# Kernel tuning notes

Measured on AMD Instinct MI355X. Metric: run time of the kernel, lower is better.

## Reference

```python
import jax, jax.numpy as jnp
import numpy as np

F = 15          # features
H = 128         # hidden_features
L = 12          # num_layers
NB = 16         # num_bins
M = 3 * NB - 1  # 47 params per feature (tails='linear')
TAIL = 3.0
MIN_W = 1e-3; MIN_H = 1e-3; MIN_D = 1e-3
B = 65536


def _masks():
    # nflows MADE sequential degrees
    deg_in = np.arange(1, F + 1)                       # input degrees 1..F
    deg_h = np.arange(H) % (F - 1) + 1                 # hidden degrees
    m_init = (deg_h[:, None] >= deg_in[None, :]).astype(np.float32)  # [H,F]
    m_h = (deg_h[:, None] >= deg_h[None, :]).astype(np.float32)      # [H,H]
    deg_out = np.repeat(deg_in, M)                     # tile -> repeat_interleave, [F*M]
    m_out = (deg_out[:, None] > deg_h[None, :]).astype(np.float32)   # [F*M,H], strict for output
    return jnp.asarray(m_init), jnp.asarray(m_h), jnp.asarray(m_out)


def setup_inputs() -> dict:
    key = jax.random.key(0)
    ks = jax.random.split(key, 7)
    s = 0.05
    return {
        "x": jax.random.normal(ks[0], (B, F), jnp.float32),
        "W_init": jax.random.normal(ks[1], (L, H, F), jnp.float32) * s,
        "b_init": jax.random.normal(ks[2], (L, H), jnp.float32) * s,
        "W_res": jax.random.normal(ks[3], (L, 2, 2, H, H), jnp.float32) * s,
        "b_res": jax.random.normal(ks[4], (L, 2, 2, H), jnp.float32) * s,
        "W_out": jax.random.normal(ks[5], (L, F * M, H), jnp.float32) * s,
        "b_out": jax.random.normal(ks[6], (L, F * M), jnp.float32) * s,
    }


def _made(x, p, m_init, m_h, m_out):
    # MADE with 2 masked residual blocks (relu, no BN/dropout), as in nflows
    h = x @ (p["W_init"] * m_init).T + p["b_init"]
    for blk in range(2):
        t = jax.nn.relu(h)
        t = t @ (p["W_res"][blk, 0] * m_h).T + p["b_res"][blk, 0]
        t = jax.nn.relu(t)
        t = t @ (p["W_res"][blk, 1] * m_h).T + p["b_res"][blk, 1]
        h = h + t
    return h @ (p["W_out"] * m_out).T + p["b_out"]  # [B, F*M]


def _rqs_forward(x, params):
    # unconstrained rational-quadratic spline, tails='linear' (nflows)
    uw = params[..., :NB]
    uh = params[..., NB:2 * NB]
    ud = params[..., 2 * NB:]                          # [B,F,NB-1]
    const = float(np.log(np.exp(1.0 - MIN_D) - 1.0))
    ud = jnp.pad(ud, ((0, 0), (0, 0), (1, 1)), constant_values=const)  # [B,F,NB+1]

    inside = (x >= -TAIL) & (x <= TAIL)
    xc = jnp.clip(x, -TAIL, TAIL)

    w = jax.nn.softmax(uw, axis=-1)
    w = MIN_W + (1.0 - MIN_W * NB) * w
    cw = jnp.pad(jnp.cumsum(w, axis=-1), ((0, 0), (0, 0), (1, 0)))
    cw = 2.0 * TAIL * cw - TAIL
    cw = cw.at[..., 0].set(-TAIL).at[..., -1].set(TAIL)
    w = cw[..., 1:] - cw[..., :-1]

    hgt = jax.nn.softmax(uh, axis=-1)
    hgt = MIN_H + (1.0 - MIN_H * NB) * hgt
    ch = jnp.pad(jnp.cumsum(hgt, axis=-1), ((0, 0), (0, 0), (1, 0)))
    ch = 2.0 * TAIL * ch - TAIL
    ch = ch.at[..., 0].set(-TAIL).at[..., -1].set(TAIL)
    hgt = ch[..., 1:] - ch[..., :-1]

    d = MIN_D + jax.nn.softplus(ud)                    # [B,F,NB+1]

    idx = jnp.clip(jnp.sum((xc[..., None] >= cw).astype(jnp.int32), axis=-1) - 1, 0, NB - 1)[..., None]
    g = lambda a: jnp.take_along_axis(a, idx, axis=-1)[..., 0]

    in_cw, in_w, in_ch, in_h = g(cw), g(w), g(ch), g(hgt)
    in_delta = g(hgt / w)
    in_d, in_d1 = g(d), g(d[..., 1:])

    theta = (xc - in_cw) / in_w
    tomt = theta * (1.0 - theta)
    num = in_h * (in_delta * theta ** 2 + in_d * tomt)
    den = in_delta + (in_d + in_d1 - 2.0 * in_delta) * tomt
    y = in_ch + num / den
    dnum = in_delta ** 2 * (in_d1 * theta ** 2 + 2.0 * in_delta * tomt + in_d * (1.0 - theta) ** 2)
    lad = jnp.log(dnum) - 2.0 * jnp.log(den)

    y = jnp.where(inside, y, x)                        # identity tails
    lad = jnp.where(inside, lad, 0.0)
    return y, jnp.sum(lad, axis=-1)


def reference(x, W_init, b_init, W_res, b_res, W_out, b_out):
    m_init, m_h, m_out = _masks()
    params = {"W_init": W_init, "b_init": b_init, "W_res": W_res,
              "b_res": b_res, "W_out": W_out, "b_out": b_out}

    def step(carry, p):
        xx, ld = carry
        xx = xx[:, ::-1]                               # ReversePermutation
        raw = _made(xx, p, m_init, m_h, m_out)
        xx, lad = _rqs_forward(xx, raw.reshape(xx.shape[0], F, M))
        return (xx, ld + lad), None

    (z, logdet), _ = jax.lax.scan(step, (x, jnp.zeros(x.shape[0], x.dtype)), params)
    return z, logdet
```

## Files before the change

kernel.cpp:

```cpp
#include <hip/hip_runtime.h>
#include <hip/hip_bf16.h>

#define FDIM 15
#define HDIM 128
#define LNUM 12
#define NBINS 16
#define MDIM 47
#define FM 705
#define BATCH 65536
#define TAILF 3.0f
#define MIN_Wc 0.001f
#define MIN_Hc 0.001f
#define MIN_Dc 0.001f

typedef __bf16 bf16_t;
typedef __attribute__((ext_vector_type(8))) __bf16 bf16x8;
typedef __attribute__((ext_vector_type(4))) __bf16 bf16x4;
typedef __attribute__((ext_vector_type(4))) float f32x4;

#define FRAGS_USED 211
#define FRAGS_PAD 224
#define FRAG_ELEMS 512
#define RING 16
#define WFRAG_TOTAL (LNUM * FRAGS_PAD * FRAG_ELEMS)

#define BB_FLOATS 1360
#define BB_TOTAL (LNUM * BB_FLOATS)

#define SPW 32

__device__ __forceinline__ int perm_pos(int pos) {
    int r, o;
    if (pos < 20) { r = pos / 10; o = pos % 10; }
    else          { r = 2 + (pos - 20) / 9; o = (pos - 20) % 9; }
    return r + 14 * o;
}

__device__ __forceinline__ float sp_softplus(float u) {
    return (u > 20.f) ? u : __logf(1.f + __expf(u));
}

__global__ void preproc_kernel(const float* __restrict__ Wi,
                               const float* __restrict__ Wr,
                               const float* __restrict__ Wo,
                               const float* __restrict__ bIg,
                               const float* __restrict__ bRg,
                               const float* __restrict__ bOg,
                               bf16_t* __restrict__ wfrag,
                               float* __restrict__ bblob) {
    const int RES_OFF[8] = {0, 1, 3, 5, 8, 11, 15, 19};
    const int OUT_OFF[15] = {0, 0, 3, 6, 9, 15, 21, 27, 36, 45, 54, 63, 75, 87, 99};
    const int OUT_CNT[15] = {0, 1, 1, 1, 2, 2, 2, 3, 3, 3, 3, 4, 4, 4, 4};

    int idx = blockIdx.x * blockDim.x + threadIdx.x;
    if (idx >= WFRAG_TOTAL) {
        int t = idx - WFRAG_TOTAL;
        if (t >= BB_TOTAL) return;
        int l = t / BB_FLOATS, r = t % BB_FLOATS;
        float v;
        if (r < 128) v = bIg[l * HDIM + perm_pos(r)];
        else if (r < 640) {
            int mat = (r - 128) >> 7, pos = (r - 128) & 127;
            v = bRg[(l * 4 + mat) * HDIM + perm_pos(pos)];
        } else {
            int q = r - 640, f = q / 48, j = q % 48;
            v = (j < 47) ? bOg[(size_t)l * FM + f * MDIM + j] : 0.f;
        }
        bblob[t] = v;
        return;
    }
    int j = idx & 7;
    int lane = (idx >> 3) & 63;
    int fg = idx >> 9;
    int g = fg % FRAGS_PAD;
    int l = fg / FRAGS_PAD;
    int quad = lane >> 4, n16 = lane & 15;
    int kk = quad * 8 + j;
    float val = 0.f;
    if (g < 8) {
        int n_orig = perm_pos(g * 16 + n16);
        if (kk < FDIM && (n_orig % 14) >= kk)
            val = Wi[(l * HDIM + n_orig) * FDIM + kk];
    } else if (g < 100) {
        int gg = g - 8;
        int mat = gg / 23, r = gg % 23;
        int mt = 7;
        while (mt > 0 && RES_OFF[mt] > r) mt--;
        int s = r - RES_OFF[mt];
        int j_orig = perm_pos(mt * 16 + n16);
        int k_orig = perm_pos(s * 32 + kk);
        if ((j_orig % 14) >= (k_orig % 14))
            val = Wr[((size_t)(l * 4 + mat) * HDIM + j_orig) * HDIM + k_orig];
    } else if (g < 211) {
        int gg = g - 100;
        int f = 14;
        while (f > 1 && OUT_OFF[f] > gg) f--;
        int q = gg - OUT_OFF[f];
        int cnt = OUT_CNT[f];
        int ty = q / cnt, s = q % cnt;
        int k_orig = perm_pos(s * 32 + kk);
        int o = (ty < 2) ? (f * MDIM + ty * 16 + n16)
                         : ((n16 < 15) ? (f * MDIM + 32 + n16) : -1);
        if (o >= 0 && f > (k_orig % 14))
            val = Wo[((size_t)l * FM + o) * HDIM + k_orig];
    }
    wfrag[idx] = (bf16_t)val;
}

__global__ __launch_bounds__(64, 2) void flow_kernel(
    const float* __restrict__ xin,
    float* __restrict__ zout,
    float* __restrict__ ldout,
    const bf16_t* __restrict__ wfrag,
    const float* __restrict__ bblob) {

    constexpr int RES_CNT_C[8] = {1, 2, 2, 3, 3, 4, 4, 4};
    constexpr int OUT_CNT_C[15] = {0, 1, 1, 1, 2, 2, 2, 3, 3, 3, 3, 4, 4, 4, 4};

    __shared__ __align__(16) float xs[SPW * 17];
    __shared__ __align__(16) unsigned char uni[13312];

    const int ln = threadIdx.x;
    const int quad = ln >> 4, n16 = ln & 15;
    const int fi = ln & 1, srow = ln >> 1;
    const int sbase = blockIdx.x * SPW;

    bf16_t* Bst = (bf16_t*)uni;
    float*  raw = (float*)uni;

    for (int t = ln; t < SPW * FDIM; t += 64) {
        int s = t / FDIM, c = t % FDIM;
        xs[s * 17 + c] = xin[(size_t)sbase * FDIM + t];
    }

    const bf16_t* wl = wfrag;
    bf16x8 Q[RING];
#pragma unroll
    for (int j = 0; j < RING; j++)
        Q[j] = *((const bf16x8*)(wl + (size_t)j * FRAG_ELEMS) + ln);

    float lad_sum = 0.f;
    bf16x8 bf[2][4];
    f32x4 h[2][8];

#pragma unroll 1
    for (int l = 0; l < LNUM; l++) {
        const float* bias = bblob + l * BB_FLOATS;

        float xc_pre[8];
#pragma unroll
        for (int p = 0; p < 8; p++) {
            int f = 2 * p + fi;
            xc_pre[p] = xs[srow * 17 + ((f < FDIM) ? (14 - f) : 0)];
        }
        bf16x8 a0[2];
#pragma unroll
        for (int T = 0; T < 2; T++)
#pragma unroll
            for (int j = 0; j < 8; j++) {
                int k = quad * 8 + j;
                a0[T][j] = (bf16_t)((k < FDIM) ? xs[(T * 16 + n16) * 17 + 14 - k] : 0.f);
            }

        int fp = 0;
        auto ldfrag = [&]() -> bf16x8 {
            bf16x8 r = Q[fp & (RING - 1)];
            Q[fp & (RING - 1)] =
                *((const bf16x8*)(wl + (size_t)(fp + RING) * FRAG_ELEMS) + ln);
            fp++;
            return r;
        };

        auto packmt = [&](int mt, f32x4 c0, f32x4 c1, bool relu) {
#pragma unroll
            for (int T = 0; T < 2; T++) {
                f32x4 c = T ? c1 : c0;
                bf16x4 pk;
#pragma unroll
                for (int r2 = 0; r2 < 4; r2++) {
                    float v = c[r2];
                    if (relu) v = fmaxf(v, 0.f);
                    pk[r2] = (bf16_t)v;
                }
                *(bf16x4*)&Bst[(T * 16 + n16) * 136 + mt * 16 + quad * 4] = pk;
            }
        };
        auto readbf = [&]() {
#pragma unroll
            for (int T = 0; T < 2; T++)
#pragma unroll
                for (int s = 0; s < 4; s++)
                    bf[T][s] = *(const bf16x8*)&Bst[(T * 16 + n16) * 136 + s * 32 + quad * 8];
        };

#pragma unroll
        for (int mt = 0; mt < 8; mt++) {
            f32x4 bbv = *(const f32x4*)&bias[mt * 16 + quad * 4];
            bf16x8 wf = ldfrag();
            f32x4 c0 = __builtin_amdgcn_mfma_f32_16x16x32_bf16(wf, a0[0], bbv, 0, 0, 0);
            f32x4 c1 = __builtin_amdgcn_mfma_f32_16x16x32_bf16(wf, a0[1], bbv, 0, 0, 0);
            h[0][mt] = c0; h[1][mt] = c1;
            packmt(mt, c0, c1, true);
        }
        readbf();

        auto gemm_pack = [&](const float* bm, bool addto, bool relu) {
#pragma unroll
            for (int mt = 0; mt < 8; mt++) {
                f32x4 bbv = *(const f32x4*)&bm[mt * 16 + quad * 4];
                f32x4 acc0 = addto ? (h[0][mt] + bbv) : bbv;
                f32x4 acc1 = addto ? (h[1][mt] + bbv) : bbv;
#pragma unroll
                for (int s = 0; s < RES_CNT_C[mt]; s++) {
                    bf16x8 wf = ldfrag();
                    acc0 = __builtin_amdgcn_mfma_f32_16x16x32_bf16(wf, bf[0][s], acc0, 0, 0, 0);
                    acc1 = __builtin_amdgcn_mfma_f32_16x16x32_bf16(wf, bf[1][s], acc1, 0, 0, 0);
                }
                if (addto) { h[0][mt] = acc0; h[1][mt] = acc1; }
                packmt(mt, acc0, acc1, relu);
            }
            readbf();
        };

        gemm_pack(bias + 128 + 0 * HDIM, false, true);
        gemm_pack(bias + 128 + 1 * HDIM, true,  true);
        gemm_pack(bias + 128 + 2 * HDIM, false, true);
        gemm_pack(bias + 128 + 3 * HDIM, true,  false);

        const float* bO48 = bias + 640;

#pragma unroll
        for (int p = 0; p < 8; p++) {
            const int nf = (p < 7) ? 2 : 1;
#pragma unroll
            for (int ff = 0; ff < 2; ff++) {
                if (ff >= nf) break;
                const int f = 2 * p + ff;
                const int cnt = OUT_CNT_C[f];
#pragma unroll
                for (int ty = 0; ty < 3; ty++) {
                    f32x4 acc0 = *(const f32x4*)&bO48[f * 48 + ty * 16 + quad * 4];
                    f32x4 acc1 = acc0;
#pragma unroll
                    for (int s = 0; s < cnt; s++) {
                        bf16x8 wf = ldfrag();
                        acc0 = __builtin_amdgcn_mfma_f32_16x16x32_bf16(wf, bf[0][s], acc0, 0, 0, 0);
                        acc1 = __builtin_amdgcn_mfma_f32_16x16x32_bf16(wf, bf[1][s], acc1, 0, 0, 0);
                    }
                    *(f32x4*)&raw[(ff * 32 + n16) * 52 + ty * 16 + quad * 4] = acc0;
                    *(f32x4*)&raw[(ff * 32 + 16 + n16) * 52 + ty * 16 + quad * 4] = acc1;
                }
            }

            if (fi < nf) {
                int f = 2 * p + fi;
                const float* rp = &raw[(fi * 32 + srow) * 52];
                float xr = xc_pre[p];
                bool inside = (xr >= -TAILF) && (xr <= TAILF);
                float xcv = fminf(fmaxf(xr, -TAILF), TAILF);

                float uw[NBINS], uh[NBINS];
                {
                    f32x4 v0 = *(const f32x4*)(rp + 0);
                    f32x4 v1 = *(const f32x4*)(rp + 4);
                    f32x4 v2 = *(const f32x4*)(rp + 8);
                    f32x4 v3 = *(const f32x4*)(rp + 12);
                    f32x4 w0 = *(const f32x4*)(rp + 16);
                    f32x4 w1 = *(const f32x4*)(rp + 20);
                    f32x4 w2 = *(const f32x4*)(rp + 24);
                    f32x4 w3 = *(const f32x4*)(rp + 28);
#pragma unroll
                    for (int i = 0; i < 4; i++) {
                        uw[i] = v0[i]; uw[4 + i] = v1[i]; uw[8 + i] = v2[i]; uw[12 + i] = v3[i];
                        uh[i] = w0[i]; uh[4 + i] = w1[i]; uh[8 + i] = w2[i]; uh[12 + i] = w3[i];
                    }
                }
                float mw = -1e30f, mh = -1e30f;
#pragma unroll
                for (int i = 0; i < NBINS; i++) {
                    mw = fmaxf(mw, uw[i]); mh = fmaxf(mh, uh[i]);
                }
                float swv = 0.f, shv = 0.f;
#pragma unroll
                for (int i = 0; i < NBINS; i++) {
                    uw[i] = __expf(uw[i] - mw); swv += uw[i];
                    uh[i] = __expf(uh[i] - mh); shv += uh[i];
                }
                float isw = (1.f - NBINS * MIN_Wc) / swv;
                float ish = (1.f - NBINS * MIN_Hc) / shv;

                float cumw = 0.f, cumh = 0.f;
                float left = -TAILF, chl_run = -TAILF;
                float lw = -TAILF, wsel = 1.f, chl = -TAILF, hsel = 1.f;
                int idx = 0;
#pragma unroll
                for (int b = 0; b < NBINS; b++) {
                    float wb = MIN_Wc + uw[b] * isw;
                    float hb = MIN_Hc + uh[b] * ish;
                    cumw += wb; cumh += hb;
                    float cwr = (b == NBINS - 1) ? TAILF : 2.f * TAILF * cumw - TAILF;
                    float chr = (b == NBINS - 1) ? TAILF : 2.f * TAILF * cumh - TAILF;
                    bool inb = (xcv >= left) && ((xcv < cwr) || (b == NBINS - 1));
                    if (inb) { idx = b; lw = left; wsel = cwr - left; chl = chl_run; hsel = chr - chl_run; }
                    left = cwr; chl_run = chr;
                }
                float d0 = 1.f, d1 = 1.f;
                if (idx > 0) d0 = MIN_Dc + sp_softplus(rp[2 * NBINS + idx - 1]);
                if (idx < NBINS - 1) d1 = MIN_Dc + sp_softplus(rp[2 * NBINS + idx]);

                float delta = hsel / wsel;
                float th = (xcv - lw) / wsel;
                float omt = 1.f - th;
                float tomt = th * omt;
                float num = hsel * (delta * th * th + d0 * tomt);
                float den = delta + (d0 + d1 - 2.f * delta) * tomt;
                float y = chl + num / den;
                float dnum = delta * delta * (d1 * th * th + 2.f * delta * tomt + d0 * omt * omt);
                float lad = __logf(dnum) - 2.f * __logf(den);

                y = inside ? y : xr;
                lad = inside ? lad : 0.f;
                xs[srow * 17 + f] = y;
                lad_sum += lad;
            }
        }

#pragma unroll
        for (int d = 0; d < FRAGS_PAD - FRAGS_USED; d++) {
            (void)ldfrag();
        }

        wl += (size_t)FRAGS_PAD * FRAG_ELEMS;
    }

    float v = lad_sum;
    v += __shfl_xor(v, 1);
    if (fi == 0) ldout[(size_t)sbase + srow] = v;

    for (int t = ln; t < SPW * FDIM; t += 64) {
        int s = t / FDIM, c = t % FDIM;
        zout[(size_t)sbase * FDIM + t] = xs[s * 17 + c];
    }
}

extern "C" void kernel_launch(void* const* d_in, const int* in_sizes, int n_in,
                              void* d_out, int out_size, void* d_ws, size_t ws_size,
                              hipStream_t stream) {
    const float* x  = (const float*)d_in[0];
    const float* Wi = (const float*)d_in[1];
    const float* bI = (const float*)d_in[2];
    const float* Wr = (const float*)d_in[3];
    const float* bR = (const float*)d_in[4];
    const float* Wo = (const float*)d_in[5];
    const float* bO = (const float*)d_in[6];

    bf16_t* wfrag = (bf16_t*)d_ws;
    size_t woff = ((size_t)WFRAG_TOTAL * 2 + (size_t)RING * FRAG_ELEMS * 2 + 255) & ~(size_t)255;
    float* bblob = (float*)((char*)d_ws + woff);
    float* zout  = (float*)d_out;
    float* ldout_final = zout + (size_t)BATCH * FDIM;

    const int totalP = WFRAG_TOTAL + BB_TOTAL;
    preproc_kernel<<<(totalP + 255) / 256, 256, 0, stream>>>(Wi, Wr, Wo, bI, bR, bO, wfrag, bblob);

    flow_kernel<<<BATCH / SPW, 64, 0, stream>>>(x, zout, ldout_final, wfrag, bblob);
}
```

Measured before the change: 413.2 us.

## Halve samples per block, shrink weight ring, and raise occupancy with 3-lane splines

Each block now handles 16 samples instead of 32. That halves the MFMA accumulator and activation registers, the weight prefetch ring shrinks from 16 to 8 fragments, and launch bounds allow 4 blocks per CU. The spline stage maps 4 lanes per sample, with 3 features per pass. Derivative parameters are preloaded into registers during bin search, and several divisions are replaced with hardware reciprocal. The aim is better latency hiding through occupancy, traded against twice the global weight-fragment traffic per sample and a shallower prefetch window.

Measured after the change: 775.2 us. 1.88x slower.

```diff
diff --git a/kernel.cpp b/kernel.cpp
--- a/kernel.cpp
+++ b/kernel.cpp
@@ -19,15 +19,18 @@
 typedef __attribute__((ext_vector_type(4))) float f32x4;
 
 #define FRAGS_USED 211
-#define FRAGS_PAD 224
+#define FRAGS_PAD 216
 #define FRAG_ELEMS 512
-#define RING 16
+#define RING 8
 #define WFRAG_TOTAL (LNUM * FRAGS_PAD * FRAG_ELEMS)
 
 #define BB_FLOATS 1360
 #define BB_TOTAL (LNUM * BB_FLOATS)
 
-#define SPW 32
+#define SPW 16
+#define RAW_ROWS 48
+#define RAW_STRIDE 52
+#define RAW_BYTES (RAW_ROWS * RAW_STRIDE * 4)
 
 __device__ __forceinline__ int perm_pos(int pos) {
     int r, o;
@@ -107,7 +110,7 @@
     wfrag[idx] = (bf16_t)val;
 }
 
-__global__ __launch_bounds__(64, 2) void flow_kernel(
+__global__ __launch_bounds__(64, 4) void flow_kernel(
     const float* __restrict__ xin,
     float* __restrict__ zout,
     float* __restrict__ ldout,
@@ -118,11 +121,11 @@
     constexpr int OUT_CNT_C[15] = {0, 1, 1, 1, 2, 2, 2, 3, 3, 3, 3, 4, 4, 4, 4};
 
     __shared__ __align__(16) float xs[SPW * 17];
-    __shared__ __align__(16) unsigned char uni[13312];
+    __shared__ __align__(16) unsigned char uni[RAW_BYTES];
 
     const int ln = threadIdx.x;
     const int quad = ln >> 4, n16 = ln & 15;
-    const int fi = ln & 1, srow = ln >> 1;
+    const int fi = ln & 3, srow = ln >> 2;
     const int sbase = blockIdx.x * SPW;
 
     bf16_t* Bst = (bf16_t*)uni;
@@ -140,27 +143,25 @@
         Q[j] = *((const bf16x8*)(wl + (size_t)j * FRAG_ELEMS) + ln);
 
     float lad_sum = 0.f;
-    bf16x8 bf[2][4];
-    f32x4 h[2][8];
+    bf16x8 bf[4];
+    f32x4 h[8];
 
 #pragma unroll 1
     for (int l = 0; l < LNUM; l++) {
         const float* bias = bblob + l * BB_FLOATS;
 
-        float xc_pre[8];
-#pragma unroll
-        for (int p = 0; p < 8; p++) {
-            int f = 2 * p + fi;
+        float xc_pre[5];
+#pragma unroll
+        for (int p = 0; p < 5; p++) {
+            int f = 3 * p + fi;
             xc_pre[p] = xs[srow * 17 + ((f < FDIM) ? (14 - f) : 0)];
         }
-        bf16x8 a0[2];
-#pragma unroll
-        for (int T = 0; T < 2; T++)
-#pragma unroll
-            for (int j = 0; j < 8; j++) {
-                int k = quad * 8 + j;
-                a0[T][j] = (bf16_t)((k < FDIM) ? xs[(T * 16 + n16) * 17 + 14 - k] : 0.f);
-            }
+        bf16x8 a0;
+#pragma unroll
+        for (int j = 0; j < 8; j++) {
+            int k = quad * 8 + j;
+            a0[j] = (bf16_t)((k < FDIM) ? xs[n16 * 17 + 14 - k] : 0.f);
+        }
 
         int fp = 0;
         auto ldfrag = [&]() -> bf16x8 {
@@ -171,36 +172,29 @@
             return r;
         };
 
-        auto packmt = [&](int mt, f32x4 c0, f32x4 c1, bool relu) {
-#pragma unroll
-            for (int T = 0; T < 2; T++) {
-                f32x4 c = T ? c1 : c0;
-                bf16x4 pk;
-#pragma unroll
-                for (int r2 = 0; r2 < 4; r2++) {
-                    float v = c[r2];
-                    if (relu) v = fmaxf(v, 0.f);
-                    pk[r2] = (bf16_t)v;
-                }
-                *(bf16x4*)&Bst[(T * 16 + n16) * 136 + mt * 16 + quad * 4] = pk;
+        auto packmt = [&](int mt, f32x4 c, bool relu) {
+            bf16x4 pk;
+#pragma unroll
+            for (int r2 = 0; r2 < 4; r2++) {
+                float v = c[r2];
+                if (relu) v = fmaxf(v, 0.f);
+                pk[r2] = (bf16_t)v;
             }
+            *(bf16x4*)&Bst[n16 * 136 + mt * 16 + quad * 4] = pk;
         };
         auto readbf = [&]() {
 #pragma unroll
-            for (int T = 0; T < 2; T++)
-#pragma unroll
-                for (int s = 0; s < 4; s++)
-                    bf[T][s] = *(const bf16x8*)&Bst[(T * 16 + n16) * 136 + s * 32 + quad * 8];
+            for (int s = 0; s < 4; s++)
+                bf[s] = *(const bf16x8*)&Bst[n16 * 136 + s * 32 + quad * 8];
         };
 
 #pragma unroll
         for (int mt = 0; mt < 8; mt++) {
             f32x4 bbv = *(const f32x4*)&bias[mt * 16 + quad * 4];
             bf16x8 wf = ldfrag();
-            f32x4 c0 = __builtin_amdgcn_mfma_f32_16x16x32_bf16(wf, a0[0], bbv, 0, 0, 0);
-            f32x4 c1 = __builtin_amdgcn_mfma_f32_16x16x32_bf16(wf, a0[1], bbv, 0, 0, 0);
-            h[0][mt] = c0; h[1][mt] = c1;
-            packmt(mt, c0, c1, true);
+            f32x4 c = __builtin_amdgcn_mfma_f32_16x16x32_bf16(wf, a0, bbv, 0, 0, 0);
+            h[mt] = c;
+            packmt(mt, c, true);
         }
         readbf();
 
@@ -208,16 +202,14 @@
 #pragma unroll
             for (int mt = 0; mt < 8; mt++) {
                 f32x4 bbv = *(const f32x4*)&bm[mt * 16 + quad * 4];
-                f32x4 acc0 = addto ? (h[0][mt] + bbv) : bbv;
-                f32x4 acc1 = addto ? (h[1][mt] + bbv) : bbv;
+                f32x4 acc = addto ? (h[mt] + bbv) : bbv;
 #pragma unroll
                 for (int s = 0; s < RES_CNT_C[mt]; s++) {
                     bf16x8 wf = ldfrag();
-                    acc0 = __builtin_amdgcn_mfma_f32_16x16x32_bf16(wf, bf[0][s], acc0, 0, 0, 0);
-                    acc1 = __builtin_amdgcn_mfma_f32_16x16x32_bf16(wf, bf[1][s], acc1, 0, 0, 0);
-                }
-                if (addto) { h[0][mt] = acc0; h[1][mt] = acc1; }
-                packmt(mt, acc0, acc1, relu);
+                    acc = __builtin_amdgcn_mfma_f32_16x16x32_bf16(wf, bf[s], acc, 0, 0, 0);
+                }
+                if (addto) h[mt] = acc;
+                packmt(mt, acc, relu);
             }
             readbf();
         };
@@ -230,36 +222,31 @@
         const float* bO48 = bias + 640;
 
 #pragma unroll
-        for (int p = 0; p < 8; p++) {
-            const int nf = (p < 7) ? 2 : 1;
-#pragma unroll
-            for (int ff = 0; ff < 2; ff++) {
-                if (ff >= nf) break;
-                const int f = 2 * p + ff;
+        for (int p = 0; p < 5; p++) {
+#pragma unroll
+            for (int ff = 0; ff < 3; ff++) {
+                const int f = 3 * p + ff;
                 const int cnt = OUT_CNT_C[f];
 #pragma unroll
                 for (int ty = 0; ty < 3; ty++) {
-                    f32x4 acc0 = *(const f32x4*)&bO48[f * 48 + ty * 16 + quad * 4];
-                    f32x4 acc1 = acc0;
+                    f32x4 acc = *(const f32x4*)&bO48[f * 48 + ty * 16 + quad * 4];
 #pragma unroll
                     for (int s = 0; s < cnt; s++) {
                         bf16x8 wf = ldfrag();
-                        acc0 = __builtin_amdgcn_mfma_f32_16x16x32_bf16(wf, bf[0][s], acc0, 0, 0, 0);
-                        acc1 = __builtin_amdgcn_mfma_f32_16x16x32_bf16(wf, bf[1][s], acc1, 0, 0, 0);
+                        acc = __builtin_amdgcn_mfma_f32_16x16x32_bf16(wf, bf[s], acc, 0, 0, 0);
                     }
-                    *(f32x4*)&raw[(ff * 32 + n16) * 52 + ty * 16 + quad * 4] = acc0;
-                    *(f32x4*)&raw[(ff * 32 + 16 + n16) * 52 + ty * 16 + quad * 4] = acc1;
+                    *(f32x4*)&raw[(ff * 16 + n16) * RAW_STRIDE + ty * 16 + quad * 4] = acc;
                 }
             }
 
-            if (fi < nf) {
-                int f = 2 * p + fi;
-                const float* rp = &raw[(fi * 32 + srow) * 52];
+            if (fi < 3) {
+                int f = 3 * p + fi;
+                const float* rp = &raw[(fi * 16 + srow) * RAW_STRIDE];
                 float xr = xc_pre[p];
                 bool inside = (xr >= -TAILF) && (xr <= TAILF);
                 float xcv = fminf(fmaxf(xr, -TAILF), TAILF);
 
-                float uw[NBINS], uh[NBINS];
+                float uw[NBINS], uh[NBINS], dval[NBINS];
                 {
                     f32x4 v0 = *(const f32x4*)(rp + 0);
                     f32x4 v1 = *(const f32x4*)(rp + 4);
@@ -269,10 +256,16 @@
                     f32x4 w1 = *(const f32x4*)(rp + 20);
                     f32x4 w2 = *(const f32x4*)(rp + 24);
                     f32x4 w3 = *(const f32x4*)(rp + 28);
+                    f32x4 d0v = *(const f32x4*)(rp + 32);
+                    f32x4 d1v = *(const f32x4*)(rp + 36);
+                    f32x4 d2v = *(const f32x4*)(rp + 40);
+                    f32x4 d3v = *(const f32x4*)(rp + 44);
 #pragma unroll
                     for (int i = 0; i < 4; i++) {
                         uw[i] = v0[i]; uw[4 + i] = v1[i]; uw[8 + i] = v2[i]; uw[12 + i] = v3[i];
                         uh[i] = w0[i]; uh[4 + i] = w1[i]; uh[8 + i] = w2[i]; uh[12 + i] = w3[i];
+                        dval[i] = d0v[i]; dval[4 + i] = d1v[i];
+                        dval[8 + i] = d2v[i]; dval[12 + i] = d3v[i];
                     }
                 }
                 float mw = -1e30f, mh = -1e30f;
@@ -286,12 +279,13 @@
                     uw[i] = __expf(uw[i] - mw); swv += uw[i];
                     uh[i] = __expf(uh[i] - mh); shv += uh[i];
                 }
-                float isw = (1.f - NBINS * MIN_Wc) / swv;
-                float ish = (1.f - NBINS * MIN_Hc) / shv;
+                float isw = (1.f - NBINS * MIN_Wc) * __builtin_amdgcn_rcpf(swv);
+                float ish = (1.f - NBINS * MIN_Hc) * __builtin_amdgcn_rcpf(shv);
 
                 float cumw = 0.f, cumh = 0.f;
                 float left = -TAILF, chl_run = -TAILF;
                 float lw = -TAILF, wsel = 1.f, chl = -TAILF, hsel = 1.f;
+                float d0r = 0.f, d1r = 0.f;
                 int idx = 0;
 #pragma unroll
                 for (int b = 0; b < NBINS; b++) {
@@ -301,20 +295,25 @@
                     float cwr = (b == NBINS - 1) ? TAILF : 2.f * TAILF * cumw - TAILF;
                     float chr = (b == NBINS - 1) ? TAILF : 2.f * TAILF * cumh - TAILF;
                     bool inb = (xcv >= left) && ((xcv < cwr) || (b == NBINS - 1));
-                    if (inb) { idx = b; lw = left; wsel = cwr - left; chl = chl_run; hsel = chr - chl_run; }
+                    if (inb) {
+                        idx = b; lw = left; wsel = cwr - left;
+                        chl = chl_run; hsel = chr - chl_run;
+                        d0r = (b > 0) ? dval[b - 1] : 0.f;
+                        d1r = (b < NBINS - 1) ? dval[b] : 0.f;
+                    }
                     left = cwr; chl_run = chr;
                 }
-                float d0 = 1.f, d1 = 1.f;
-                if (idx > 0) d0 = MIN_Dc + sp_softplus(rp[2 * NBINS + idx - 1]);
-                if (idx < NBINS - 1) d1 = MIN_Dc + sp_softplus(rp[2 * NBINS + idx]);
-
-                float delta = hsel / wsel;
-                float th = (xcv - lw) / wsel;
+                float d0 = (idx > 0) ? (MIN_Dc + sp_softplus(d0r)) : 1.f;
+                float d1 = (idx < NBINS - 1) ? (MIN_Dc + sp_softplus(d1r)) : 1.f;
+
+                float rw = __builtin_amdgcn_rcpf(wsel);
+                float delta = hsel * rw;
+                float th = (xcv - lw) * rw;
                 float omt = 1.f - th;
                 float tomt = th * omt;
                 float num = hsel * (delta * th * th + d0 * tomt);
                 float den = delta + (d0 + d1 - 2.f * delta) * tomt;
-                float y = chl + num / den;
+                float y = chl + num * __builtin_amdgcn_rcpf(den);
                 float dnum = delta * delta * (d1 * th * th + 2.f * delta * tomt + d0 * omt * omt);
                 float lad = __logf(dnum) - 2.f * __logf(den);
 
@@ -335,6 +334,7 @@
 
     float v = lad_sum;
     v += __shfl_xor(v, 1);
+    v += __shfl_xor(v, 2);
     if (fi == 0) ldout[(size_t)sbase + srow] = v;
 
     for (int t = ln; t < SPW * FDIM; t += 64) {
```

## Transpose MFMA outputs to B-operand layout via ds_bpermute instead of LDS staging

Applied to the files above, without the earlier changes.

Replaces the LDS write/read round trip that converted each hidden layer's MFMA accumulator layout into the next GEMM's B-operand fragments with in-register lane shuffles using ds_bpermute. Pairs of 16-row tiles are packed to bf16x2 and gathered into bf16x8 fragments, and the LDS buffer shrinks to hold only the raw output tile. This removes LDS stores, the reads after them and the implicit waits between GEMMs. In exchange it issues eight bpermutes per fragment plus selects, and adds register pressure from the bfn array.

New measurement: 437.5 us. 5.9% more time.

```diff
diff --git a/kernel.cpp b/kernel.cpp
--- a/kernel.cpp
+++ b/kernel.cpp
@@ -16,7 +16,9 @@
 typedef __bf16 bf16_t;
 typedef __attribute__((ext_vector_type(8))) __bf16 bf16x8;
 typedef __attribute__((ext_vector_type(4))) __bf16 bf16x4;
+typedef __attribute__((ext_vector_type(2))) __bf16 bf16x2;
 typedef __attribute__((ext_vector_type(4))) float f32x4;
+typedef __attribute__((ext_vector_type(4))) int i32x4;
 
 #define FRAGS_USED 211
 #define FRAGS_PAD 224
@@ -118,15 +120,39 @@
     constexpr int OUT_CNT_C[15] = {0, 1, 1, 1, 2, 2, 2, 3, 3, 3, 3, 4, 4, 4, 4};
 
     __shared__ __align__(16) float xs[SPW * 17];
-    __shared__ __align__(16) unsigned char uni[13312];
+    __shared__ __align__(16) float raw[64 * 52];
 
     const int ln = threadIdx.x;
     const int quad = ln >> 4, n16 = ln & 15;
     const int fi = ln & 1, srow = ln >> 1;
     const int sbase = blockIdx.x * SPW;
 
-    bf16_t* Bst = (bf16_t*)uni;
-    float*  raw = (float*)uni;
+    const int l0lane = ((ln >> 4) & 1) * 32 + (ln & 15);
+    const int idx0 = l0lane << 2;
+    const int idx1 = idx0 + 64;
+    const bool hi = (ln >= 32);
+
+    auto pack2 = [&](float a, float b, bool relu) -> int {
+        if (relu) { a = fmaxf(a, 0.f); b = fmaxf(b, 0.f); }
+        bf16x2 t; t[0] = (bf16_t)a; t[1] = (bf16_t)b;
+        return __builtin_bit_cast(int, t);
+    };
+    auto gath4 = [&](int e01, int e23, int o01, int o23) -> bf16x8 {
+        int a0_ = __builtin_amdgcn_ds_bpermute(idx0, e01);
+        int b0_ = __builtin_amdgcn_ds_bpermute(idx0, o01);
+        int a1_ = __builtin_amdgcn_ds_bpermute(idx0, e23);
+        int b1_ = __builtin_amdgcn_ds_bpermute(idx0, o23);
+        int a2_ = __builtin_amdgcn_ds_bpermute(idx1, e01);
+        int b2_ = __builtin_amdgcn_ds_bpermute(idx1, o01);
+        int a3_ = __builtin_amdgcn_ds_bpermute(idx1, e23);
+        int b3_ = __builtin_amdgcn_ds_bpermute(idx1, o23);
+        i32x4 d;
+        d[0] = hi ? b0_ : a0_;
+        d[1] = hi ? b1_ : a1_;
+        d[2] = hi ? b2_ : a2_;
+        d[3] = hi ? b3_ : a3_;
+        return __builtin_bit_cast(bf16x8, d);
+    };
 
     for (int t = ln; t < SPW * FDIM; t += 64) {
         int s = t / FDIM, c = t % FDIM;
@@ -141,6 +167,7 @@
 
     float lad_sum = 0.f;
     bf16x8 bf[2][4];
+    bf16x8 bfn[2][4];
     f32x4 h[2][8];
 
 #pragma unroll 1
@@ -171,40 +198,32 @@
             return r;
         };
 
-        auto packmt = [&](int mt, f32x4 c0, f32x4 c1, bool relu) {
-#pragma unroll
-            for (int T = 0; T < 2; T++) {
-                f32x4 c = T ? c1 : c0;
-                bf16x4 pk;
-#pragma unroll
-                for (int r2 = 0; r2 < 4; r2++) {
-                    float v = c[r2];
-                    if (relu) v = fmaxf(v, 0.f);
-                    pk[r2] = (bf16_t)v;
-                }
-                *(bf16x4*)&Bst[(T * 16 + n16) * 136 + mt * 16 + quad * 4] = pk;
-            }
-        };
-        auto readbf = [&]() {
+        {
+            int pe01_0, pe23_0, pe01_1, pe23_1;
+#pragma unroll
+            for (int mt = 0; mt < 8; mt++) {
+                f32x4 bbv = *(const f32x4*)&bias[mt * 16 + quad * 4];
+                bf16x8 wf = ldfrag();
+                f32x4 c0 = __builtin_amdgcn_mfma_f32_16x16x32_bf16(wf, a0[0], bbv, 0, 0, 0);
+                f32x4 c1 = __builtin_amdgcn_mfma_f32_16x16x32_bf16(wf, a0[1], bbv, 0, 0, 0);
+                h[0][mt] = c0; h[1][mt] = c1;
+                int p01_0 = pack2(c0[0], c0[1], true), p23_0 = pack2(c0[2], c0[3], true);
+                int p01_1 = pack2(c1[0], c1[1], true), p23_1 = pack2(c1[2], c1[3], true);
+                if (!(mt & 1)) { pe01_0 = p01_0; pe23_0 = p23_0; pe01_1 = p01_1; pe23_1 = p23_1; }
+                else {
+                    int s2 = mt >> 1;
+                    bfn[0][s2] = gath4(pe01_0, pe23_0, p01_0, p23_0);
+                    bfn[1][s2] = gath4(pe01_1, pe23_1, p01_1, p23_1);
+                }
+            }
 #pragma unroll
             for (int T = 0; T < 2; T++)
 #pragma unroll
-                for (int s = 0; s < 4; s++)
-                    bf[T][s] = *(const bf16x8*)&Bst[(T * 16 + n16) * 136 + s * 32 + quad * 8];
-        };
-
-#pragma unroll
-        for (int mt = 0; mt < 8; mt++) {
-            f32x4 bbv = *(const f32x4*)&bias[mt * 16 + quad * 4];
-            bf16x8 wf = ldfrag();
-            f32x4 c0 = __builtin_amdgcn_mfma_f32_16x16x32_bf16(wf, a0[0], bbv, 0, 0, 0);
-            f32x4 c1 = __builtin_amdgcn_mfma_f32_16x16x32_bf16(wf, a0[1], bbv, 0, 0, 0);
-            h[0][mt] = c0; h[1][mt] = c1;
-            packmt(mt, c0, c1, true);
-        }
-        readbf();
+                for (int s = 0; s < 4; s++) bf[T][s] = bfn[T][s];
+        }
 
         auto gemm_pack = [&](const float* bm, bool addto, bool relu) {
+            int pe01_0, pe23_0, pe01_1, pe23_1;
 #pragma unroll
             for (int mt = 0; mt < 8; mt++) {
                 f32x4 bbv = *(const f32x4*)&bm[mt * 16 + quad * 4];
@@ -217,9 +236,19 @@
                     acc1 = __builtin_amdgcn_mfma_f32_16x16x32_bf16(wf, bf[1][s], acc1, 0, 0, 0);
                 }
                 if (addto) { h[0][mt] = acc0; h[1][mt] = acc1; }
-                packmt(mt, acc0, acc1, relu);
-            }
-            readbf();
+                int p01_0 = pack2(acc0[0], acc0[1], relu), p23_0 = pack2(acc0[2], acc0[3], relu);
+                int p01_1 = pack2(acc1[0], acc1[1], relu), p23_1 = pack2(acc1[2], acc1[3], relu);
+                if (!(mt & 1)) { pe01_0 = p01_0; pe23_0 = p23_0; pe01_1 = p01_1; pe23_1 = p23_1; }
+                else {
+                    int s2 = mt >> 1;
+                    bfn[0][s2] = gath4(pe01_0, pe23_0, p01_0, p23_0);
+                    bfn[1][s2] = gath4(pe01_1, pe23_1, p01_1, p23_1);
+                }
+            }
+#pragma unroll
+            for (int T = 0; T < 2; T++)
+#pragma unroll
+                for (int s = 0; s < 4; s++) bf[T][s] = bfn[T][s];
         };
 
         gemm_pack(bias + 128 + 0 * HDIM, false, true);
```
